# Kernel optimization log

Measured on AMD Instinct MI355X. Metric: run time of the kernel, lower is better.

The kernel has to match this reference:

```python
import jax, jax.numpy as jnp
import numpy as np

N = 100000      # nodes
E = 3200000     # edges
IN = 64         # in_channels
OUT = 256       # out_channels (hidden)
OSZ = 4         # output_size


def setup_inputs() -> dict:
    key = jax.random.key(0)
    ks = jax.random.split(key, 16)
    s = 0.05
    inp = {
        "x": jax.random.normal(ks[0], (N, IN), jnp.float32),
        "edge_index": jax.random.randint(ks[1], (2, E), 0, N, jnp.int64),
        # GCNConv weights for z, r, h gates: [IN, OUT] + bias [OUT]
        "Wz": jax.random.normal(ks[2], (IN, OUT), jnp.float32) * s,
        "bz": jnp.zeros((OUT,), jnp.float32),
        "Wr": jax.random.normal(ks[3], (IN, OUT), jnp.float32) * s,
        "br": jnp.zeros((OUT,), jnp.float32),
        "Wh": jax.random.normal(ks[4], (IN, OUT), jnp.float32) * s,
        "bh": jnp.zeros((OUT,), jnp.float32),
        # GRU linear layers: [2*OUT, OUT] + bias [OUT]
        "Lzw": jax.random.normal(ks[5], (2 * OUT, OUT), jnp.float32) * s,
        "Lzb": jnp.zeros((OUT,), jnp.float32),
        "Lrw": jax.random.normal(ks[6], (2 * OUT, OUT), jnp.float32) * s,
        "Lrb": jnp.zeros((OUT,), jnp.float32),
        "Lhw": jax.random.normal(ks[7], (2 * OUT, OUT), jnp.float32) * s,
        "Lhb": jnp.zeros((OUT,), jnp.float32),
        # output head
        "Wo": jax.random.normal(ks[8], (OUT, OSZ), jnp.float32) * s,
        "bo": jnp.zeros((OSZ,), jnp.float32),
    }
    return inp


def _gcn_conv(x, W, b, src, dst, n):
    # GCNConv with symmetric normalization and self-loops (fill_value=1):
    # out = D^{-1/2}(A+I)D^{-1/2} X W + b
    ones = jnp.ones_like(src, dtype=x.dtype)
    deg = jax.ops.segment_sum(ones, dst, num_segments=n) + 1.0  # +1 for self-loop
    dinv = jax.lax.rsqrt(deg)                                   # [N]
    norm = dinv[src] * dinv[dst]                                # [E]
    agg = jax.ops.segment_sum(x[src] * norm[:, None], dst, num_segments=n)
    agg = agg + x * (dinv * dinv)[:, None]                      # self-loop term
    return agg @ W + b


def reference(x, edge_index, Wz, bz, Wr, br, Wh, bh,
              Lzw, Lzb, Lrw, Lrb, Lhw, Lhb, Wo, bo):
    src, dst = edge_index[0], edge_index[1]
    n = x.shape[0]
    H = jnp.zeros((n, Wz.shape[1]), x.dtype)  # TGCN initial hidden state
    # update gate
    Z = jax.nn.sigmoid(jnp.concatenate([_gcn_conv(x, Wz, bz, src, dst, n), H], 1) @ Lzw + Lzb)
    # reset gate
    R = jax.nn.sigmoid(jnp.concatenate([_gcn_conv(x, Wr, br, src, dst, n), H], 1) @ Lrw + Lrb)
    # candidate state
    Ht = jnp.tanh(jnp.concatenate([_gcn_conv(x, Wh, bh, src, dst, n), H * R], 1) @ Lhw + Lhb)
    H = Z * H + (1.0 - Z) * Ht
    # head: ReLU -> Linear -> Softmax(dim=1)
    h = jax.nn.relu(H)
    return jax.nn.softmax(h @ Wo + bo, axis=1)
```

## Files before the change

### kernel.cpp

```cpp
#include <hip/hip_runtime.h>
#include <hip/hip_fp16.h>


#define SHIFT 8
#define NPB   256
#define BMAX  512
#define TILE  8192
#define MBBLK 64
#define CAP   7936
#define CAPB  9216

typedef __attribute__((ext_vector_type(8))) short short8;
typedef __attribute__((ext_vector_type(4))) float floatx4;

__device__ __forceinline__ ushort f2b(float f) {
    union { float f; unsigned u; } v; v.f = f;
    unsigned r = v.u + 0x7FFFu + ((v.u >> 16) & 1u);
    return (ushort)(r >> 16);
}

__device__ __forceinline__ float fastrcp(float x) {
    return __builtin_amdgcn_rcpf(x);
}

__global__ __launch_bounds__(512) void scatter_build_kernel(
    const int* __restrict__ srcs, const int* __restrict__ dsts,
    int* __restrict__ gcur, int* __restrict__ staging, int E, int B, int nT,
    const float* __restrict__ Wz, const float* __restrict__ bz,
    const float* __restrict__ Wh, const float* __restrict__ bh,
    const float* __restrict__ Lzw, const float* __restrict__ Lzb,
    const float* __restrict__ Lhw, const float* __restrict__ Lhb,
    ushort* __restrict__ Mb, float* __restrict__ cb) {
    __shared__ int h[BMAX];
    if (blockIdx.x < nT) {
        int tid = threadIdx.x;
        for (int i = tid; i < B; i += 512) h[i] = 0;
        __syncthreads();
        int tile0 = blockIdx.x * TILE;
#pragma unroll 4
        for (int j = 0; j < TILE / 512; ++j) {
            int e = tile0 + j * 512 + tid;
            if (e < E) atomicAdd(&h[((unsigned)dsts[e]) >> SHIFT], 1);
        }
        __syncthreads();
        for (int i = tid; i < B; i += 512) {
            int c = h[i];
            h[i] = (c > 0) ? atomicAdd(&gcur[i], c) : 0;
        }
        __syncthreads();
#pragma unroll 4
        for (int j = 0; j < TILE / 512; ++j) {
            int e = tile0 + j * 512 + tid;
            if (e < E) {
                int d = dsts[e], s = srcs[e];
                int b = ((unsigned)d) >> SHIFT;
                int pos = atomicAdd(&h[b], 1);
                if (pos < CAPB)
                    staging[(size_t)b * CAPB + pos] = ((d & (NPB - 1)) << 17) | s;
            }
        }
    } else {
        int j = (blockIdx.x - nT) * 8 + (threadIdx.x >> 6);
        int k = threadIdx.x & 63;
        int which = j >> 8;
        int jj = j & 255;
        const float* W  = which ? Wh  : Wz;
        const float* bv = which ? bh  : bz;
        const float* L  = which ? Lhw : Lzw;
        const float* Lb = which ? Lhb : Lzb;
        float acc = 0.f;
        for (int t = 0; t < 256; ++t) acc = fmaf(W[k * 256 + t], L[t * 256 + jj], acc);
        Mb[j * 64 + k] = f2b(acc);
        if (k == 0) {
            float a = 0.f;
            for (int t = 0; t < 256; ++t) a = fmaf(bv[t], L[t * 256 + jj], a);
            cb[j] = a + Lb[jj];
        }
    }
}

__global__ __launch_bounds__(512) void prep_kernel(const int* __restrict__ staging,
                                                   const int* __restrict__ gcur,
                                                   const float* __restrict__ x,
                                                   int* __restrict__ deg,
                                                   __half* __restrict__ xs,
                                                   int n, int B) {
    int b = blockIdx.x;
    int tid = threadIdx.x;
    __shared__ int nd[NPB];
    __shared__ float sdinv[NPB];
    if (tid < NPB) nd[tid] = 0;
    __syncthreads();
    int count = gcur[b];
    if (count > CAPB) count = CAPB;
    size_t base = (size_t)b * CAPB;
    for (int i = tid; i < count; i += 512)
        atomicAdd(&nd[staging[base + i] >> 17], 1);
    __syncthreads();
    if (tid < NPB) {
        int dg = nd[tid];
        float dn = rsqrtf((float)dg + 1.0f);
        sdinv[tid] = dn;
        int node = (b << SHIFT) + tid;
        if (node < n) deg[node] = dg;
    }
    __syncthreads();
    int nbase = b << SHIFT;
    for (int i2 = tid; i2 < NPB * 16; i2 += 512) {
        int nl = i2 >> 4;
        int node = nbase + nl;
        if (node < n) {
            float dn = sdinv[nl];
            size_t gi = (size_t)node * 16 + (i2 & 15);
            float4 vx = ((const float4*)x)[gi];
            __half2 a = __floats2half2_rn(vx.x * dn, vx.y * dn);
            __half2 c = __floats2half2_rn(vx.z * dn, vx.w * dn);
            ((__half2*)xs)[gi * 2 + 0] = a;
            ((__half2*)xs)[gi * 2 + 1] = c;
        }
    }
}

__global__ __launch_bounds__(512) void bucket_gather_kernel(
    const int* __restrict__ staging,
    const int* __restrict__ gcur,
    const int* __restrict__ deg,
    const __half* __restrict__ xs,
    ushort* __restrict__ aggb, int n, int B) {
    int b    = blockIdx.x >> 1;
    int half = blockIdx.x & 1;
    int tid  = threadIdx.x;
    __shared__ int   csrl[CAP];
    __shared__ int   sstart[128];
    __shared__ int   ncur[128];
    __shared__ int   sdeg[128];
    __shared__ int   ssc[128];
    __shared__ float sdinv[128];
    int node0 = (b << SHIFT) + (half << 7);
    int count = gcur[b];
    if (count > CAPB) count = CAPB;
    size_t base = (size_t)b * CAPB;
    if (tid < 128) {
        int nodeid = node0 + tid;
        int dg = (nodeid < n) ? deg[nodeid] : 0;
        sdeg[tid] = dg;
        ssc[tid]  = dg;
        sdinv[tid] = rsqrtf((float)dg + 1.0f);
    }
    __syncthreads();
    for (int off = 1; off < 128; off <<= 1) {
        int t = 0;
        if (tid < 128 && tid >= off) t = ssc[tid - off];
        __syncthreads();
        if (tid < 128) ssc[tid] += t;
        __syncthreads();
    }
    if (tid < 128) {
        int excl = ssc[tid] - sdeg[tid];
        sstart[tid] = excl;
        ncur[tid]   = excl;
    }
    __syncthreads();
    for (int i = tid; i < count; i += 512) {
        int p  = staging[base + i];
        int dl = p >> 17;
        if ((dl >> 7) == half) {
            int pos = atomicAdd(&ncur[dl & 127], 1);
            if (pos < CAP) csrl[pos] = p & 0x1FFFF;
        }
    }
    __syncthreads();
    int wv = tid >> 6, lane = tid & 63;
    int eg = lane >> 3;
    int c  = lane & 7;
    for (int t16 = 0; t16 < 16; ++t16) {
        int nl   = (wv << 4) + t16;
        int node = node0 + nl;
        int s0 = sstart[nl];
        int d  = sdeg[nl];
        __half2 hz = __float2half2_rn(0.f);
        __half2 hacc[4] = {hz, hz, hz, hz};
        int full = d & ~15;
        for (int be = 0; be < full; be += 16) {
            int qb = s0 + be;
            if (qb > CAP - 16) qb = CAP - 16;
            int i0 = csrl[qb + eg];
            int i1 = csrl[qb + 8 + eg];
            union { uint4 u; __half2 h[4]; } p0, p1;
            p0.u = *(const uint4*)(xs + (size_t)i0 * 64 + c * 8);
            p1.u = *(const uint4*)(xs + (size_t)i1 * 64 + c * 8);
#pragma unroll
            for (int t = 0; t < 4; ++t) hacc[t] = __hadd2(hacc[t], p0.h[t]);
#pragma unroll
            for (int t = 0; t < 4; ++t) hacc[t] = __hadd2(hacc[t], p1.h[t]);
        }
        if (full < d) {
            int e0 = full + eg;
            int e1 = full + 8 + eg;
            int q0 = s0 + (e0 < d ? e0 : d - 1);
            int q1 = s0 + (e1 < d ? e1 : d - 1);
            if (q0 > CAP - 1) q0 = CAP - 1;
            if (q1 > CAP - 1) q1 = CAP - 1;
            int i0 = csrl[q0];
            int i1 = csrl[q1];
            union { uint4 u; __half2 h[4]; } p0, p1;
            p0.u = *(const uint4*)(xs + (size_t)i0 * 64 + c * 8);
            p1.u = *(const uint4*)(xs + (size_t)i1 * 64 + c * 8);
            if (e0 >= d) p0.u = make_uint4(0u, 0u, 0u, 0u);
            if (e1 >= d) p1.u = make_uint4(0u, 0u, 0u, 0u);
#pragma unroll
            for (int t = 0; t < 4; ++t) hacc[t] = __hadd2(hacc[t], p0.h[t]);
#pragma unroll
            for (int t = 0; t < 4; ++t) hacc[t] = __hadd2(hacc[t], p1.h[t]);
        }
#pragma unroll
        for (int off = 32; off >= 8; off >>= 1) {
#pragma unroll
            for (int t = 0; t < 4; ++t) {
                union { __half2 h; int i; } u;
                u.h = hacc[t];
                u.i = __shfl_down(u.i, off);
                hacc[t] = __hadd2(hacc[t], u.h);
            }
        }
        if (eg == 0 && node < n) {
            float dn = sdinv[nl];
            union { uint4 u; __half2 h[4]; } p;
            p.u = *(const uint4*)(xs + (size_t)node * 64 + c * 8);
            uint4 o;
            unsigned* ow = (unsigned*)&o;
#pragma unroll
            for (int t = 0; t < 4; ++t) {
                float2 a = __half22float2(hacc[t]);
                float2 f = __half22float2(p.h[t]);
                float v0 = dn * fmaf(f.x, dn, a.x);
                float v1 = dn * fmaf(f.y, dn, a.y);
                ow[t] = (unsigned)f2b(v0) | ((unsigned)f2b(v1) << 16);
            }
            ((uint4*)(aggb + (size_t)node * 64))[c] = o;
        }
    }
}

__global__ __launch_bounds__(512) void node_mfma_kernel(
    const ushort* __restrict__ aggb,
    const ushort* __restrict__ Mb,
    const float* __restrict__ cb,
    const float* __restrict__ Wo, const float* __restrict__ bo,
    float* __restrict__ out, int n) {
    int tid  = threadIdx.x;
    int w    = tid >> 6;
    int lane = tid & 63;
    int nidx = lane & 15;
    int quad = lane >> 4;
    short8 bfz[2][2], bfh[2][2];
    float cbz[2], cbh[2];
#pragma unroll
    for (int cg = 0; cg < 2; ++cg) {
        int colZ = (w << 5) + (cg << 4) + nidx;
        int colH = 256 + colZ;
#pragma unroll
        for (int s = 0; s < 2; ++s) {
            bfz[cg][s] = *(const short8*)(Mb + colZ * 64 + s * 32 + quad * 8);
            bfh[cg][s] = *(const short8*)(Mb + colH * 64 + s * 32 + quad * 8);
        }
        cbz[cg] = cb[colZ];
        cbh[cg] = cb[colH];
    }
    __shared__ float sH[32][260];
    __shared__ float sWo[4][256];
    if (tid < 256) {
#pragma unroll
        for (int o = 0; o < 4; ++o) sWo[o][tid] = Wo[tid * 4 + o];
    }
    float bo0 = bo[0], bo1 = bo[1], bo2 = bo[2], bo3 = bo[3];
    int ntiles = (n + 31) >> 5;
    for (int tile = blockIdx.x; tile < ntiles; tile += gridDim.x) {
        int node0 = tile << 5;
        int nA0 = node0 + nidx;
        int nA1 = node0 + 16 + nidx;
        if (nA0 >= n) nA0 = n - 1;
        if (nA1 >= n) nA1 = n - 1;
        const ushort* ar0 = aggb + (size_t)nA0 * 64;
        const ushort* ar1 = aggb + (size_t)nA1 * 64;
        short8 a00 = *(const short8*)(ar0 + quad * 8);
        short8 a01 = *(const short8*)(ar0 + 32 + quad * 8);
        short8 a10 = *(const short8*)(ar1 + quad * 8);
        short8 a11 = *(const short8*)(ar1 + 32 + quad * 8);
#pragma unroll
        for (int cg = 0; cg < 2; ++cg) {
            int col = (w << 5) + (cg << 4) + nidx;
#pragma unroll
            for (int grp = 0; grp < 2; ++grp) {
                short8 a0 = grp ? a10 : a00;
                short8 a1 = grp ? a11 : a01;
                floatx4 cz = {cbz[cg], cbz[cg], cbz[cg], cbz[cg]};
                cz = __builtin_amdgcn_mfma_f32_16x16x32_bf16(a0, bfz[cg][0], cz, 0, 0, 0);
                cz = __builtin_amdgcn_mfma_f32_16x16x32_bf16(a1, bfz[cg][1], cz, 0, 0, 0);
                floatx4 chh = {cbh[cg], cbh[cg], cbh[cg], cbh[cg]};
                chh = __builtin_amdgcn_mfma_f32_16x16x32_bf16(a0, bfh[cg][0], chh, 0, 0, 0);
                chh = __builtin_amdgcn_mfma_f32_16x16x32_bf16(a1, bfh[cg][1], chh, 0, 0, 0);
#pragma unroll
                for (int r = 0; r < 4; ++r) {
                    int row = (grp << 4) + (quad << 2) + r;
                    float zc = fastrcp(1.0f + __expf(cz[r]));
                    float th = 1.0f - 2.0f * fastrcp(1.0f + __expf(2.0f * chh[r]));
                    sH[row][col] = fmaxf(zc * th, 0.0f);
                }
            }
        }
        __syncthreads();
        {
            int nb = tid >> 4, g = tid & 15;
            float l0 = 0.f, l1 = 0.f, l2 = 0.f, l3 = 0.f;
#pragma unroll
            for (int ii = 0; ii < 16; ++ii) {
                int ch = g + 16 * ii;
                float hv = sH[nb][ch];
                l0 = fmaf(hv, sWo[0][ch], l0);
                l1 = fmaf(hv, sWo[1][ch], l1);
                l2 = fmaf(hv, sWo[2][ch], l2);
                l3 = fmaf(hv, sWo[3][ch], l3);
            }
#pragma unroll
            for (int off = 8; off > 0; off >>= 1) {
                l0 += __shfl_down(l0, off, 16);
                l1 += __shfl_down(l1, off, 16);
                l2 += __shfl_down(l2, off, 16);
                l3 += __shfl_down(l3, off, 16);
            }
            int node = node0 + nb;
            if (g == 0 && node < n) {
                float v0 = l0 + bo0, v1 = l1 + bo1, v2 = l2 + bo2, v3 = l3 + bo3;
                float mx = fmaxf(fmaxf(v0, v1), fmaxf(v2, v3));
                float e0 = __expf(v0 - mx), e1 = __expf(v1 - mx);
                float e2 = __expf(v2 - mx), e3 = __expf(v3 - mx);
                float inv = fastrcp(e0 + e1 + e2 + e3);
                float4 o;
                o.x = e0 * inv; o.y = e1 * inv; o.z = e2 * inv; o.w = e3 * inv;
                ((float4*)out)[node] = o;
            }
        }
        __syncthreads();
    }
}

extern "C" void kernel_launch(void* const* d_in, const int* in_sizes, int n_in,
                              void* d_out, int out_size, void* d_ws, size_t ws_size,
                              hipStream_t stream) {
    const float* x   = (const float*)d_in[0];
    const int*  eidx = (const int*)d_in[1];
    const float* Wz  = (const float*)d_in[2];
    const float* bz  = (const float*)d_in[3];
    const float* Wh  = (const float*)d_in[6];
    const float* bh  = (const float*)d_in[7];
    const float* Lzw = (const float*)d_in[8];
    const float* Lzb = (const float*)d_in[9];
    const float* Lhw = (const float*)d_in[12];
    const float* Lhb = (const float*)d_in[13];
    const float* Wo  = (const float*)d_in[14];
    const float* bo  = (const float*)d_in[15];
    float* out = (float*)d_out;

    int n = in_sizes[0] / 64;
    int E = in_sizes[1] / 2;
    const int* srcs = eidx;
    const int* dsts = eidx + E;
    int B = (n + NPB - 1) >> SHIFT;
    int nT = (E + TILE - 1) / TILE;

    size_t na = ((size_t)n + 3) & ~(size_t)3;
    size_t stageBytes = (((size_t)B * CAPB * 4) + 255) & ~(size_t)255;
    size_t aggBytes   = (((size_t)n * 64 * 2) + 255) & ~(size_t)255;

    char* ws = (char*)d_ws;
    int*   deg   = (int*)ws;    ws += na * 4;
    int*   gcur  = (int*)ws;    ws += BMAX * 4;
    int*   staging = (int*)ws;  ws += stageBytes;
    __half* xs   = (__half*)ws; ws += (size_t)n * 64 * 2;
    ushort* aggb = (ushort*)ws; ws += aggBytes;
    ushort* Mb   = (ushort*)ws; ws += 512 * 64 * 2;
    float* cb    = (float*)ws;  ws += 512 * 4;

    hipMemsetAsync(gcur, 0, BMAX * 4, stream);
    scatter_build_kernel<<<nT + MBBLK, 512, 0, stream>>>(srcs, dsts, gcur,
                                                         staging, E, B, nT,
                                                         Wz, bz, Wh, bh,
                                                         Lzw, Lzb, Lhw, Lhb,
                                                         Mb, cb);
    prep_kernel<<<B, 512, 0, stream>>>(staging, gcur, x, deg, xs, n, B);
    bucket_gather_kernel<<<2 * B, 512, 0, stream>>>(staging, gcur, deg,
                                                    xs, aggb, n, B);
    node_mfma_kernel<<<1024, 512, 0, stream>>>(aggb, Mb, cb, Wo, bo, out, n);
}
```

Before: 252.1 us.

## Sort edges per tile in shared memory and halve bucket size

The scatter kernel now counting-sorts each tile's edges by bucket in shared memory and writes every bucket's run contiguously with wave-cooperative stores, instead of scattering each edge straight to global staging. Buckets shrink to 128 nodes, so the gather kernel runs one block per bucket and no longer reads the staging data twice with half of it discarded. The aim is coalesced staging writes and half the staging reads. The cost is a 1024-entry prefix scan per tile, more shared memory in the scatter kernel that may lower occupancy, and per-bucket capacity that assumes in-degree stays bounded.

```diff
diff --git a/kernel.cpp b/kernel.cpp
--- a/kernel.cpp
+++ b/kernel.cpp
@@ -2,13 +2,13 @@
 #include <hip/hip_fp16.h>
 
 
-#define SHIFT 8
-#define NPB   256
-#define BMAX  512
+#define SHIFT 7
+#define NPB   128
+#define BMAX  1024
 #define TILE  8192
+#define EPT   16
 #define MBBLK 64
-#define CAP   7936
-#define CAPB  9216
+#define CAPB  5120
 
 typedef __attribute__((ext_vector_type(8))) short short8;
 typedef __attribute__((ext_vector_type(4))) float floatx4;
@@ -31,33 +31,65 @@
     const float* __restrict__ Lzw, const float* __restrict__ Lzb,
     const float* __restrict__ Lhw, const float* __restrict__ Lhb,
     ushort* __restrict__ Mb, float* __restrict__ cb) {
-    __shared__ int h[BMAX];
+    __shared__ int cnt[BMAX];
+    __shared__ int ssum[BMAX];
+    __shared__ int gbase[BMAX];
+    __shared__ int cur[BMAX];
+    __shared__ int sorted[TILE];
     if (blockIdx.x < nT) {
         int tid = threadIdx.x;
-        for (int i = tid; i < B; i += 512) h[i] = 0;
+        for (int i = tid; i < BMAX; i += 512) cnt[i] = 0;
         __syncthreads();
         int tile0 = blockIdx.x * TILE;
-#pragma unroll 4
-        for (int j = 0; j < TILE / 512; ++j) {
+        int dreg[EPT];
+#pragma unroll
+        for (int j = 0; j < EPT; ++j) {
             int e = tile0 + j * 512 + tid;
-            if (e < E) atomicAdd(&h[((unsigned)dsts[e]) >> SHIFT], 1);
-        }
-        __syncthreads();
-        for (int i = tid; i < B; i += 512) {
-            int c = h[i];
-            h[i] = (c > 0) ? atomicAdd(&gcur[i], c) : 0;
-        }
-        __syncthreads();
-#pragma unroll 4
-        for (int j = 0; j < TILE / 512; ++j) {
-            int e = tile0 + j * 512 + tid;
-            if (e < E) {
-                int d = dsts[e], s = srcs[e];
+            dreg[j] = (e < E) ? dsts[e] : -1;
+            if (dreg[j] >= 0) atomicAdd(&cnt[((unsigned)dreg[j]) >> SHIFT], 1);
+        }
+        __syncthreads();
+        {
+            int i0 = tid, i1 = tid + 512;
+            ssum[i0] = cnt[i0];
+            ssum[i1] = cnt[i1];
+            __syncthreads();
+            for (int off = 1; off < BMAX; off <<= 1) {
+                int t0 = (i0 >= off) ? ssum[i0 - off] : 0;
+                int t1 = (i1 >= off) ? ssum[i1 - off] : 0;
+                __syncthreads();
+                ssum[i0] += t0;
+                ssum[i1] += t1;
+                __syncthreads();
+            }
+        }
+        for (int i = tid; i < BMAX; i += 512) {
+            int c = cnt[i];
+            gbase[i] = (c > 0) ? atomicAdd(&gcur[i], c) : 0;
+            cur[i] = ssum[i] - c;
+        }
+        __syncthreads();
+#pragma unroll
+        for (int j = 0; j < EPT; ++j) {
+            int d = dreg[j];
+            if (d >= 0) {
+                int e = tile0 + j * 512 + tid;
+                int s = srcs[e];
                 int b = ((unsigned)d) >> SHIFT;
-                int pos = atomicAdd(&h[b], 1);
-                if (pos < CAPB)
-                    staging[(size_t)b * CAPB + pos] = ((d & (NPB - 1)) << 17) | s;
-            }
+                int pos = atomicAdd(&cur[b], 1);
+                sorted[pos] = ((d & (NPB - 1)) << 17) | s;
+            }
+        }
+        __syncthreads();
+        int wv = tid >> 6, lane = tid & 63;
+        for (int b = wv; b < B; b += 8) {
+            int c = cnt[b];
+            if (c == 0) continue;
+            int lb = ssum[b] - c;
+            int gb = gbase[b];
+            size_t gp = (size_t)b * CAPB + gb;
+            for (int j = lane; j < c; j += 64)
+                if (gb + j < CAPB) staging[gp + j] = sorted[lb + j];
         }
     } else {
         int j = (blockIdx.x - nT) * 8 + (threadIdx.x >> 6);
@@ -127,20 +159,19 @@
     const int* __restrict__ deg,
     const __half* __restrict__ xs,
     ushort* __restrict__ aggb, int n, int B) {
-    int b    = blockIdx.x >> 1;
-    int half = blockIdx.x & 1;
-    int tid  = threadIdx.x;
-    __shared__ int   csrl[CAP];
-    __shared__ int   sstart[128];
-    __shared__ int   ncur[128];
-    __shared__ int   sdeg[128];
-    __shared__ int   ssc[128];
-    __shared__ float sdinv[128];
-    int node0 = (b << SHIFT) + (half << 7);
+    int b   = blockIdx.x;
+    int tid = threadIdx.x;
+    __shared__ int   csrl[CAPB];
+    __shared__ int   sstart[NPB];
+    __shared__ int   ncur[NPB];
+    __shared__ int   sdeg[NPB];
+    __shared__ int   ssc[NPB];
+    __shared__ float sdinv[NPB];
+    int node0 = b << SHIFT;
     int count = gcur[b];
     if (count > CAPB) count = CAPB;
     size_t base = (size_t)b * CAPB;
-    if (tid < 128) {
+    if (tid < NPB) {
         int nodeid = node0 + tid;
         int dg = (nodeid < n) ? deg[nodeid] : 0;
         sdeg[tid] = dg;
@@ -148,26 +179,23 @@
         sdinv[tid] = rsqrtf((float)dg + 1.0f);
     }
     __syncthreads();
-    for (int off = 1; off < 128; off <<= 1) {
+    for (int off = 1; off < NPB; off <<= 1) {
         int t = 0;
-        if (tid < 128 && tid >= off) t = ssc[tid - off];
-        __syncthreads();
-        if (tid < 128) ssc[tid] += t;
-        __syncthreads();
-    }
-    if (tid < 128) {
+        if (tid < NPB && tid >= off) t = ssc[tid - off];
+        __syncthreads();
+        if (tid < NPB) ssc[tid] += t;
+        __syncthreads();
+    }
+    if (tid < NPB) {
         int excl = ssc[tid] - sdeg[tid];
         sstart[tid] = excl;
         ncur[tid]   = excl;
     }
     __syncthreads();
     for (int i = tid; i < count; i += 512) {
-        int p  = staging[base + i];
-        int dl = p >> 17;
-        if ((dl >> 7) == half) {
-            int pos = atomicAdd(&ncur[dl & 127], 1);
-            if (pos < CAP) csrl[pos] = p & 0x1FFFF;
-        }
+        int p = staging[base + i];
+        int pos = atomicAdd(&ncur[p >> 17], 1);
+        if (pos < CAPB) csrl[pos] = p & 0x1FFFF;
     }
     __syncthreads();
     int wv = tid >> 6, lane = tid & 63;
@@ -183,7 +211,7 @@
         int full = d & ~15;
         for (int be = 0; be < full; be += 16) {
             int qb = s0 + be;
-            if (qb > CAP - 16) qb = CAP - 16;
+            if (qb > CAPB - 16) qb = CAPB - 16;
             int i0 = csrl[qb + eg];
             int i1 = csrl[qb + 8 + eg];
             union { uint4 u; __half2 h[4]; } p0, p1;
@@ -199,8 +227,8 @@
             int e1 = full + 8 + eg;
             int q0 = s0 + (e0 < d ? e0 : d - 1);
             int q1 = s0 + (e1 < d ? e1 : d - 1);
-            if (q0 > CAP - 1) q0 = CAP - 1;
-            if (q1 > CAP - 1) q1 = CAP - 1;
+            if (q0 > CAPB - 1) q0 = CAPB - 1;
+            if (q1 > CAPB - 1) q1 = CAPB - 1;
             int i0 = csrl[q0];
             int i1 = csrl[q1];
             union { uint4 u; __half2 h[4]; } p0, p1;
@@ -389,7 +417,7 @@
                                                          Lzw, Lzb, Lhw, Lhb,
                                                          Mb, cb);
     prep_kernel<<<B, 512, 0, stream>>>(staging, gcur, x, deg, xs, n, B);
-    bucket_gather_kernel<<<2 * B, 512, 0, stream>>>(staging, gcur, deg,
-                                                    xs, aggb, n, B);
+    bucket_gather_kernel<<<B, 512, 0, stream>>>(staging, gcur, deg,
+                                                xs, aggb, n, B);
     node_mfma_kernel<<<1024, 512, 0, stream>>>(aggb, Mb, cb, Wo, bo, out, n);
 }
```

Measured after the change: 249.5 us. Within noise of the previous version (-1.0%).
